# Kernel optimization log

Hardware: AMD Instinct MI355X
Metric: run time of the kernel (lower is better)

Reference implementation:

```python
import math
import jax, jax.numpy as jnp
import numpy as np

N = 8192
IN_DIM = 256
OUT_DIM = 128


def setup_inputs() -> dict:
    key = jax.random.key(0)
    k_feat, k_c, k_q, k_k, k_v = jax.random.split(key, 5)
    feat = jax.random.normal(k_feat, (N, IN_DIM), dtype=jnp.float32)
    counting_attn = jax.random.uniform(k_c, (N, N), dtype=jnp.float32)
    # Linear weights stored as [in_dim, out_dim] (x @ W == nn.Linear with W.T)
    Wq = jax.random.normal(k_q, (IN_DIM, OUT_DIM), dtype=jnp.float32) / math.sqrt(IN_DIM)
    Wk = jax.random.normal(k_k, (IN_DIM, OUT_DIM), dtype=jnp.float32) / math.sqrt(IN_DIM)
    Wv = jax.random.normal(k_v, (IN_DIM, OUT_DIM), dtype=jnp.float32) / math.sqrt(IN_DIM)
    return {"feat": feat, "bg": 0, "counting_attn": counting_attn,
            "Wq": Wq, "Wk": Wk, "Wv": Wv}


def reference(feat, bg, counting_attn, Wq, Wk, Wv):
    # bg (graph handle) is unused in the original forward; dropout prob = 0.
    Q = feat @ Wq                      # [N, D]
    K = feat @ Wk                      # [N, D]
    V = feat @ Wv                      # [N, D]
    scale = 1.0 / math.sqrt(Q.shape[1])
    logits = (Q @ K.T) * scale         # [N, N]
    logits = logits - jnp.max(logits, axis=1, keepdims=True)
    a_nomi = jnp.exp(logits) @ counting_attn          # [N, N]
    a_deno = jnp.sum(a_nomi, axis=1, keepdims=True)
    a_nor = a_nomi / (a_deno + 1e-9)
    ret = a_nor @ V                    # [N, D]
    return jax.nn.elu(ret)
```

## Files before the change

kernel.cpp:

```cpp
#include <hip/hip_runtime.h>


typedef __attribute__((ext_vector_type(8))) short bf16x8;
typedef __attribute__((ext_vector_type(4))) short bf16x4;
typedef __attribute__((ext_vector_type(4))) float f32x4;

#define SC2 (0.088388347648318447f * 1.4426950408889634f)

static __device__ __forceinline__ unsigned short f2bf(float f) {
    unsigned u = __float_as_uint(f);
    u = (u + 0x7fffu + ((u >> 16) & 1u)) >> 16;
    return (unsigned short)u;
}
static __device__ __forceinline__ float bf2f(unsigned short b) {
    return __uint_as_float(((unsigned)b) << 16);
}
static __device__ __forceinline__ unsigned pkbf(float lo, float hi) {
    unsigned r;
    asm("v_cvt_pk_bf16_f32 %0, %1, %2" : "=v"(r) : "v"(lo), "v"(hi));
    return r;
}
static __device__ __forceinline__ float fexp2(float x) {
    float r;
    asm("v_exp_f32 %0, %1" : "=v"(r) : "v"(x));
    return r;
}
static __device__ __forceinline__ bf16x8 pack8(const float4& a, const float4& b) {
    union { unsigned u[4]; bf16x8 v; } o;
    o.u[0] = pkbf(a.x, a.y); o.u[1] = pkbf(a.z, a.w);
    o.u[2] = pkbf(b.x, b.y); o.u[3] = pkbf(b.z, b.w);
    return o.v;
}
static __device__ __forceinline__ void gl_lds16(const unsigned short* g, unsigned short* l) {
    __builtin_amdgcn_global_load_lds(
        (const __attribute__((address_space(1))) unsigned int*)g,
        (__attribute__((address_space(3))) unsigned int*)l, 16, 0, 0);
}

__global__ __launch_bounds__(512) void qkv_mfma(
    const float* __restrict__ feat, const float* __restrict__ Wq,
    const float* __restrict__ Wk, const float* __restrict__ Wv,
    unsigned short* __restrict__ Qb, unsigned short* __restrict__ Kb,
    unsigned short* __restrict__ VbT, float* __restrict__ qn2,
    unsigned* __restrict__ knmax) {
    __shared__ unsigned short As[64][264];
    __shared__ unsigned short Bs[128][264];
    __shared__ float sn[2][64];
    const int tid = threadIdx.x;
    const int m0 = blockIdx.x * 64;
    const int mat = blockIdx.y;
    const float* W = (mat == 0) ? Wq : (mat == 1) ? Wk : Wv;
    const int lane = tid & 63, wv = tid >> 6;
    const int wm = wv & 3, wn = wv >> 2;
    const int ln15 = lane & 15, quad = lane >> 4;

    #pragma unroll
    for (int i = 0; i < 4; i++) {
        int s = tid + i * 512;
        int r = s >> 5, c8 = s & 31;
        const float* p = feat + (size_t)(m0 + r) * 256 + c8 * 8;
        const float4 f0 = *(const float4*)p;
        const float4 f1 = *(const float4*)(p + 4);
        *(bf16x8*)&As[r][c8 * 8] = pack8(f0, f1);
    }
    #pragma unroll
    for (int i = 0; i < 16; i++) {
        int s = tid + i * 512;
        int k = s >> 5, n4 = (s & 31) * 4;
        const float4 f = *(const float4*)(W + (size_t)k * 128 + n4);
        Bs[n4 + 0][k] = f2bf(f.x); Bs[n4 + 1][k] = f2bf(f.y);
        Bs[n4 + 2][k] = f2bf(f.z); Bs[n4 + 3][k] = f2bf(f.w);
    }
    __syncthreads();

    f32x4 acc[4];
    #pragma unroll
    for (int t = 0; t < 4; t++) acc[t] = f32x4{0.f, 0.f, 0.f, 0.f};
    #pragma unroll
    for (int ks = 0; ks < 8; ks++) {
        bf16x8 af = *(const bf16x8*)&As[wm * 16 + ln15][ks * 32 + quad * 8];
        #pragma unroll
        for (int t = 0; t < 4; t++) {
            bf16x8 bf = *(const bf16x8*)&Bs[wn * 64 + t * 16 + ln15][ks * 32 + quad * 8];
            acc[t] = __builtin_amdgcn_mfma_f32_16x16x32_bf16(af, bf, acc[t], 0, 0, 0);
        }
    }
    #pragma unroll
    for (int t = 0; t < 4; t++) {
        int n = wn * 64 + t * 16 + ln15;
        int mb = m0 + wm * 16 + quad * 4;
        if (mat == 2) {
            uint2 w;
            w.x = pkbf(acc[t][0], acc[t][1]);
            w.y = pkbf(acc[t][2], acc[t][3]);
            *(uint2*)(VbT + (size_t)n * 8192 + mb) = w;
        } else {
            unsigned short* dst = (mat == 0) ? Qb : Kb;
            #pragma unroll
            for (int reg = 0; reg < 4; reg++)
                dst[(size_t)(mb + reg) * 128 + n] = f2bf(acc[t][reg]);
        }
    }
    if (mat == 2) {
        #pragma unroll
        for (int i = 0; i < 8; i++) {
            int idx = tid + i * 512;
            int rr = idx >> 6, c = idx & 63;
            VbT[(size_t)(128 + rr) * 8192 + m0 + c] =
                (rr == 0) ? (unsigned short)0x3F80 : (unsigned short)0;
        }
    } else {
        float s[4];
        #pragma unroll
        for (int reg = 0; reg < 4; reg++) {
            float x = acc[0][reg] * acc[0][reg] + acc[1][reg] * acc[1][reg]
                    + acc[2][reg] * acc[2][reg] + acc[3][reg] * acc[3][reg];
            #pragma unroll
            for (int m = 1; m < 16; m <<= 1) x += __shfl_xor(x, m, 64);
            s[reg] = x;
        }
        if (ln15 == 0) {
            #pragma unroll
            for (int reg = 0; reg < 4; reg++)
                sn[wn][wm * 16 + quad * 4 + reg] = s[reg];
        }
        __syncthreads();
        if (tid < 64) {
            float tot = sn[0][tid] + sn[1][tid];
            if (mat == 0) {
                qn2[m0 + tid] = tot;
            } else {
                #pragma unroll
                for (int m = 1; m < 64; m <<= 1)
                    tot = fmaxf(tot, __shfl_xor(tot, m, 64));
                if (tid == 0) atomicMax(knmax, __float_as_uint(tot));
            }
        }
    }
}

__global__ __launch_bounds__(256, 4) void cv_kernel(
    const float* __restrict__ C, const unsigned short* __restrict__ VbT,
    float* __restrict__ CVpart) {
    __shared__ unsigned short As[64 * 64];
    __shared__ unsigned short Bs[192 * 64];
    const int tid = threadIdx.x;
    const int rg = blockIdx.x >> 3, sp = blockIdx.x & 7;
    const int m0 = rg * 64;
    const int k0 = sp * 1024;
    const int lane = tid & 63, wv = tid >> 6;
    const int mh = wv & 1, h2 = wv >> 1;
    const int ln15 = lane & 15, quad = lane >> 4;

    const int r0 = tid >> 3, gc = tid & 7;
    const int gsw = gc ^ (r0 & 7);
    const float* A0 = C + (size_t)(m0 + r0) * 8192 + k0 + gc * 8;
    const float* A1 = A0 + (size_t)32 * 8192;

    float4 pa[4];
    pa[0] = *(const float4*)A0; pa[1] = *(const float4*)(A0 + 4);
    pa[2] = *(const float4*)A1; pa[3] = *(const float4*)(A1 + 4);

    f32x4 acc[2][5];
    #pragma unroll
    for (int mt = 0; mt < 2; mt++)
        #pragma unroll
        for (int t = 0; t < 5; t++) acc[mt][t] = f32x4{0.f, 0.f, 0.f, 0.f};

    const int ra0 = mh * 32 + ln15;
    const int ra1 = mh * 32 + 16 + ln15;

    for (int c = 0; c < 16; c++) {
        __syncthreads();
        *(bf16x8*)&As[r0 * 64 + gsw * 8]        = pack8(pa[0], pa[1]);
        *(bf16x8*)&As[(r0 + 32) * 64 + gsw * 8] = pack8(pa[2], pa[3]);
        #pragma unroll
        for (int i = 0; i < 6; i++) {
            int s = (i * 4 + wv) * 64 + lane;
            int r = s >> 3, g = (s & 7) ^ (r & 7);
            gl_lds16(VbT + (size_t)r * 8192 + k0 + c * 64 + g * 8,
                     &Bs[(i * 4 + wv) * 512]);
        }
        asm volatile("" ::: "memory");
        if (c + 1 < 16) {
            const float* p0 = A0 + (c + 1) * 64;
            const float* p1 = A1 + (c + 1) * 64;
            pa[0] = *(const float4*)p0; pa[1] = *(const float4*)(p0 + 4);
            pa[2] = *(const float4*)p1; pa[3] = *(const float4*)(p1 + 4);
            asm volatile("s_waitcnt vmcnt(4) lgkmcnt(0)" ::: "memory");
        } else {
            asm volatile("s_waitcnt vmcnt(0) lgkmcnt(0)" ::: "memory");
        }
        __builtin_amdgcn_s_barrier();
        __builtin_amdgcn_sched_barrier(0);
        #pragma unroll
        for (int k2 = 0; k2 < 2; k2++) {
            const int lg = k2 * 4 + quad;
            bf16x8 a0 = *(const bf16x8*)&As[ra0 * 64 + ((lg ^ (ra0 & 7)) * 8)];
            bf16x8 a1 = *(const bf16x8*)&As[ra1 * 64 + ((lg ^ (ra1 & 7)) * 8)];
            #pragma unroll
            for (int t = 0; t < 5; t++) {
                int n = h2 * 80 + t * 16 + ln15;
                bf16x8 bf = *(const bf16x8*)&Bs[n * 64 + ((lg ^ (n & 7)) * 8)];
                acc[0][t] = __builtin_amdgcn_mfma_f32_16x16x32_bf16(a0, bf, acc[0][t], 0, 0, 0);
                acc[1][t] = __builtin_amdgcn_mfma_f32_16x16x32_bf16(a1, bf, acc[1][t], 0, 0, 0);
            }
        }
    }
    float* dst = CVpart + (size_t)sp * 160 * 8192;
    #pragma unroll
    for (int mt = 0; mt < 2; mt++)
        #pragma unroll
        for (int t = 0; t < 5; t++) {
            int n = h2 * 80 + t * 16 + ln15;
            int m = m0 + mh * 32 + mt * 16 + quad * 4;
            float4 w;
            w.x = acc[mt][t][0]; w.y = acc[mt][t][1];
            w.z = acc[mt][t][2]; w.w = acc[mt][t][3];
            *(float4*)(dst + (size_t)n * 8192 + m) = w;
        }
}

__global__ __launch_bounds__(256) void cvreduce_kernel(
    const float* __restrict__ CVpart, unsigned short* __restrict__ CVbT) {
    const size_t STR = (size_t)160 * 8192;
    int idx = blockIdx.x * 256 + threadIdx.x;
    const float* p = CVpart + (size_t)idx * 4;
    float4 s = *(const float4*)p;
    #pragma unroll
    for (int j = 1; j < 8; j++) {
        const float4 q = *(const float4*)(p + j * STR);
        s.x += q.x; s.y += q.y; s.z += q.z; s.w += q.w;
    }
    uint2 w;
    w.x = pkbf(s.x, s.y); w.y = pkbf(s.z, s.w);
    *(uint2*)(CVbT + (size_t)idx * 4) = w;
}

__global__ __launch_bounds__(256, 2) void flash_kernel(
    const unsigned short* __restrict__ Qb, const unsigned short* __restrict__ Kb,
    const unsigned short* __restrict__ CVbT, const float* __restrict__ qn2,
    const unsigned* __restrict__ knmax, float* __restrict__ Opart) {
    __shared__ unsigned short Ks[64 * 128];
    __shared__ unsigned short Cs[160 * 64];
    __shared__ unsigned short Ps[64][68];
    const int tid = threadIdx.x;
    const int rg = blockIdx.x >> 2, sp = blockIdx.x & 3;
    const int i0 = rg * 64;
    const int k0 = sp * 2048;
    const int lane = tid & 63, wv = tid >> 6;
    const int ln15 = lane & 15, quad = lane >> 4;
    const int p2 = wv & 1;
    const int h2 = wv >> 1;

    bf16x8 qf[2][4];
    #pragma unroll
    for (int mt = 0; mt < 2; mt++)
        #pragma unroll
        for (int kk = 0; kk < 4; kk++) {
            int row = i0 + p2 * 32 + mt * 16 + ln15;
            qf[mt][kk] = *(const bf16x8*)(Qb + (size_t)row * 128 + kk * 32 + quad * 8);
        }
    const float kn2 = __uint_as_float(*knmax);
    float Msr[2][4];
    #pragma unroll
    for (int mt = 0; mt < 2; mt++)
        #pragma unroll
        for (int reg = 0; reg < 4; reg++) {
            int row = p2 * 32 + mt * 16 + quad * 4 + reg;
            Msr[mt][reg] = sqrtf(qn2[i0 + row] * kn2) * SC2;
        }

    f32x4 acc[2][5];
    #pragma unroll
    for (int mt = 0; mt < 2; mt++)
        #pragma unroll
        for (int t = 0; t < 5; t++) acc[mt][t] = f32x4{0.f, 0.f, 0.f, 0.f};

    #pragma unroll
    for (int i = 0; i < 4; i++) {
        int s = (i * 4 + wv) * 64 + lane;
        int r = s >> 4, g = (s & 15) ^ (r & 15);
        gl_lds16(Kb + (size_t)(k0 + r) * 128 + g * 8, &Ks[(i * 4 + wv) * 512]);
    }

    for (int c = 0; c < 32; c++) {
        const int kb = k0 + c * 64;
        asm volatile("s_waitcnt vmcnt(0) lgkmcnt(0)" ::: "memory");
        __builtin_amdgcn_s_barrier();
        __builtin_amdgcn_sched_barrier(0);

        #pragma unroll
        for (int i = 0; i < 5; i++) {
            int s = (i * 4 + wv) * 64 + lane;
            int r = s >> 3, g = (s & 7) ^ (r & 7);
            gl_lds16(CVbT + (size_t)r * 8192 + kb + g * 8, &Cs[(i * 4 + wv) * 512]);
        }
        __builtin_amdgcn_sched_barrier(0);

        f32x4 pacc[2][2];
        #pragma unroll
        for (int mt = 0; mt < 2; mt++)
            #pragma unroll
            for (int kt = 0; kt < 2; kt++) pacc[mt][kt] = f32x4{0.f, 0.f, 0.f, 0.f};
        #pragma unroll
        for (int kk = 0; kk < 4; kk++) {
            #pragma unroll
            for (int kt = 0; kt < 2; kt++) {
                int r = h2 * 32 + kt * 16 + ln15;
                int lg = kk * 4 + quad;
                bf16x8 bk = *(const bf16x8*)&Ks[r * 128 + ((lg ^ (r & 15)) * 8)];
                pacc[0][kt] = __builtin_amdgcn_mfma_f32_16x16x32_bf16(qf[0][kk], bk, pacc[0][kt], 0, 0, 0);
                pacc[1][kt] = __builtin_amdgcn_mfma_f32_16x16x32_bf16(qf[1][kk], bk, pacc[1][kt], 0, 0, 0);
            }
        }
        #pragma unroll
        for (int mt = 0; mt < 2; mt++)
            #pragma unroll
            for (int kt = 0; kt < 2; kt++) {
                int key = h2 * 32 + kt * 16 + ln15;
                int row0 = p2 * 32 + mt * 16 + quad * 4;
                float e0 = fexp2(pacc[mt][kt][0] * SC2 - Msr[mt][0]);
                float e1 = fexp2(pacc[mt][kt][1] * SC2 - Msr[mt][1]);
                float e2 = fexp2(pacc[mt][kt][2] * SC2 - Msr[mt][2]);
                float e3 = fexp2(pacc[mt][kt][3] * SC2 - Msr[mt][3]);
                unsigned p01 = pkbf(e0, e1), p23 = pkbf(e2, e3);
                Ps[row0 + 0][key] = (unsigned short)(p01 & 0xffffu);
                Ps[row0 + 1][key] = (unsigned short)(p01 >> 16);
                Ps[row0 + 2][key] = (unsigned short)(p23 & 0xffffu);
                Ps[row0 + 3][key] = (unsigned short)(p23 >> 16);
            }

        asm volatile("s_waitcnt vmcnt(0) lgkmcnt(0)" ::: "memory");
        __builtin_amdgcn_s_barrier();
        __builtin_amdgcn_sched_barrier(0);

        if (c + 1 < 32) {
            const int kb2 = k0 + (c + 1) * 64;
            #pragma unroll
            for (int i = 0; i < 4; i++) {
                int s = (i * 4 + wv) * 64 + lane;
                int r = s >> 4, g = (s & 15) ^ (r & 15);
                gl_lds16(Kb + (size_t)(kb2 + r) * 128 + g * 8, &Ks[(i * 4 + wv) * 512]);
            }
        }
        __builtin_amdgcn_sched_barrier(0);

        #pragma unroll
        for (int ks = 0; ks < 2; ks++) {
            bf16x4 lo0 = *(const bf16x4*)&Ps[p2 * 32 + ln15][ks * 32 + quad * 8];
            bf16x4 hi0 = *(const bf16x4*)&Ps[p2 * 32 + ln15][ks * 32 + quad * 8 + 4];
            bf16x4 lo1 = *(const bf16x4*)&Ps[p2 * 32 + 16 + ln15][ks * 32 + quad * 8];
            bf16x4 hi1 = *(const bf16x4*)&Ps[p2 * 32 + 16 + ln15][ks * 32 + quad * 8 + 4];
            bf16x8 ap0, ap1;
            #pragma unroll
            for (int j = 0; j < 4; j++) {
                ap0[j] = lo0[j]; ap0[j + 4] = hi0[j];
                ap1[j] = lo1[j]; ap1[j + 4] = hi1[j];
            }
            #pragma unroll
            for (int t = 0; t < 5; t++) {
                int n = h2 * 80 + t * 16 + ln15;
                int lg = ks * 4 + quad;
                bf16x8 bc = *(const bf16x8*)&Cs[n * 64 + ((lg ^ (n & 7)) * 8)];
                acc[0][t] = __builtin_amdgcn_mfma_f32_16x16x32_bf16(ap0, bc, acc[0][t], 0, 0, 0);
                acc[1][t] = __builtin_amdgcn_mfma_f32_16x16x32_bf16(ap1, bc, acc[1][t], 0, 0, 0);
            }
        }
    }
    float* dst = Opart + (size_t)sp * 8192 * 160;
    #pragma unroll
    for (int mt = 0; mt < 2; mt++)
        #pragma unroll
        for (int t = 0; t < 5; t++)
            #pragma unroll
            for (int reg = 0; reg < 4; reg++) {
                int row = i0 + p2 * 32 + mt * 16 + quad * 4 + reg;
                int n = h2 * 80 + t * 16 + ln15;
                dst[(size_t)row * 160 + n] = acc[mt][t][reg];
            }
}

__global__ __launch_bounds__(256) void finalize_kernel(
    const float* __restrict__ Opart, float* __restrict__ out) {
    const size_t STR = (size_t)8192 * 160;
    int idx = blockIdx.x * 256 + threadIdx.x;
    int i = idx >> 7, n = idx & 127;
    const float* p = Opart + (size_t)i * 160;
    float val = 0.f, deno = 0.f;
    #pragma unroll
    for (int sp = 0; sp < 4; sp++) {
        val  += p[sp * STR + n];
        deno += p[sp * STR + 128];
    }
    float v = val / (deno + 1e-9f);
    out[idx] = (v > 0.f) ? v : expm1f(v);
}

extern "C" void kernel_launch(void* const* d_in, const int* in_sizes, int n_in,
                              void* d_out, int out_size, void* d_ws, size_t ws_size,
                              hipStream_t stream) {
    const float* feat = (const float*)d_in[0];
    const float* C    = (const float*)d_in[2];
    const float* Wq   = (const float*)d_in[3];
    const float* Wk   = (const float*)d_in[4];
    const float* Wv   = (const float*)d_in[5];
    float* out = (float*)d_out;

    char* ws = (char*)d_ws;
    unsigned short* Qb    = (unsigned short*)(ws + 0);
    unsigned short* Kb    = (unsigned short*)(ws + 2097152);
    unsigned short* VbT   = (unsigned short*)(ws + 4194304);
    float*          CVpart= (float*)(ws + 7340032);
    unsigned short* CVbT  = (unsigned short*)(ws + 49283072);
    float*          Opart = (float*)(ws + 51904512);
    float*          qn2   = (float*)(ws + 93847552);
    unsigned*       knmax = (unsigned*)(ws + 93880320);

    hipMemsetAsync(knmax, 0, 4, stream);
    qkv_mfma<<<dim3(128, 3), 512, 0, stream>>>(feat, Wq, Wk, Wv, Qb, Kb, VbT, qn2, knmax);
    cv_kernel<<<1024, 256, 0, stream>>>(C, VbT, CVpart);
    cvreduce_kernel<<<1280, 256, 0, stream>>>(CVpart, CVbT);
    flash_kernel<<<512, 256, 0, stream>>>(Qb, Kb, CVbT, qn2, knmax, Opart);
    finalize_kernel<<<4096, 256, 0, stream>>>(Opart, out);
}
```

Baseline: 486.8 us.

## Retile CV GEMM to 32-row blocks with 2-way split-K; transpose P tile in flash

The C·V kernel now uses 32-row tiles with a 2-way K split instead of 64 rows with an 8-way split. This shrinks the partial buffer and the reduction to two reads per element, but each block now reloads the V^T tile for fewer rows, and there are fewer blocks and less MFMA work per LDS load. Separately, the flash kernel swaps the MFMA operands so each lane holds one query row's scores. P can then be written with packed 64-bit swizzled LDS stores and read back as two 64-bit loads, instead of scattered 16-bit stores and element shuffles.

```diff
diff --git a/kernel.cpp b/kernel.cpp
--- a/kernel.cpp
+++ b/kernel.cpp
@@ -2,7 +2,6 @@
 
 
 typedef __attribute__((ext_vector_type(8))) short bf16x8;
-typedef __attribute__((ext_vector_type(4))) short bf16x4;
 typedef __attribute__((ext_vector_type(4))) float f32x4;
 
 #define SC2 (0.088388347648318447f * 1.4426950408889634f)
@@ -11,9 +10,6 @@
     unsigned u = __float_as_uint(f);
     u = (u + 0x7fffu + ((u >> 16) & 1u)) >> 16;
     return (unsigned short)u;
-}
-static __device__ __forceinline__ float bf2f(unsigned short b) {
-    return __uint_as_float(((unsigned)b) << 16);
 }
 static __device__ __forceinline__ unsigned pkbf(float lo, float hi) {
     unsigned r;
@@ -139,15 +135,15 @@
     }
 }
 
-__global__ __launch_bounds__(256, 4) void cv_kernel(
+__global__ __launch_bounds__(256, 2) void cv_kernel(
     const float* __restrict__ C, const unsigned short* __restrict__ VbT,
     float* __restrict__ CVpart) {
-    __shared__ unsigned short As[64 * 64];
+    __shared__ unsigned short As[32 * 64];
     __shared__ unsigned short Bs[192 * 64];
     const int tid = threadIdx.x;
-    const int rg = blockIdx.x >> 3, sp = blockIdx.x & 7;
-    const int m0 = rg * 64;
-    const int k0 = sp * 1024;
+    const int rg = blockIdx.x >> 1, sp = blockIdx.x & 1;
+    const int m0 = rg * 32;
+    const int k0 = sp * 4096;
     const int lane = tid & 63, wv = tid >> 6;
     const int mh = wv & 1, h2 = wv >> 1;
     const int ln15 = lane & 15, quad = lane >> 4;
@@ -155,25 +151,19 @@
     const int r0 = tid >> 3, gc = tid & 7;
     const int gsw = gc ^ (r0 & 7);
     const float* A0 = C + (size_t)(m0 + r0) * 8192 + k0 + gc * 8;
-    const float* A1 = A0 + (size_t)32 * 8192;
-
-    float4 pa[4];
+
+    float4 pa[2];
     pa[0] = *(const float4*)A0; pa[1] = *(const float4*)(A0 + 4);
-    pa[2] = *(const float4*)A1; pa[3] = *(const float4*)(A1 + 4);
-
-    f32x4 acc[2][5];
-    #pragma unroll
-    for (int mt = 0; mt < 2; mt++)
-        #pragma unroll
-        for (int t = 0; t < 5; t++) acc[mt][t] = f32x4{0.f, 0.f, 0.f, 0.f};
-
-    const int ra0 = mh * 32 + ln15;
-    const int ra1 = mh * 32 + 16 + ln15;
-
-    for (int c = 0; c < 16; c++) {
+
+    f32x4 acc[5];
+    #pragma unroll
+    for (int t = 0; t < 5; t++) acc[t] = f32x4{0.f, 0.f, 0.f, 0.f};
+
+    const int ra = mh * 16 + ln15;
+
+    for (int c = 0; c < 64; c++) {
         __syncthreads();
-        *(bf16x8*)&As[r0 * 64 + gsw * 8]        = pack8(pa[0], pa[1]);
-        *(bf16x8*)&As[(r0 + 32) * 64 + gsw * 8] = pack8(pa[2], pa[3]);
+        *(bf16x8*)&As[r0 * 64 + gsw * 8] = pack8(pa[0], pa[1]);
         #pragma unroll
         for (int i = 0; i < 6; i++) {
             int s = (i * 4 + wv) * 64 + lane;
@@ -182,12 +172,10 @@
                      &Bs[(i * 4 + wv) * 512]);
         }
         asm volatile("" ::: "memory");
-        if (c + 1 < 16) {
+        if (c + 1 < 64) {
             const float* p0 = A0 + (c + 1) * 64;
-            const float* p1 = A1 + (c + 1) * 64;
             pa[0] = *(const float4*)p0; pa[1] = *(const float4*)(p0 + 4);
-            pa[2] = *(const float4*)p1; pa[3] = *(const float4*)(p1 + 4);
-            asm volatile("s_waitcnt vmcnt(4) lgkmcnt(0)" ::: "memory");
+            asm volatile("s_waitcnt vmcnt(2) lgkmcnt(0)" ::: "memory");
         } else {
             asm volatile("s_waitcnt vmcnt(0) lgkmcnt(0)" ::: "memory");
         }
@@ -196,29 +184,25 @@
         #pragma unroll
         for (int k2 = 0; k2 < 2; k2++) {
             const int lg = k2 * 4 + quad;
-            bf16x8 a0 = *(const bf16x8*)&As[ra0 * 64 + ((lg ^ (ra0 & 7)) * 8)];
-            bf16x8 a1 = *(const bf16x8*)&As[ra1 * 64 + ((lg ^ (ra1 & 7)) * 8)];
+            bf16x8 a = *(const bf16x8*)&As[ra * 64 + ((lg ^ (ra & 7)) * 8)];
             #pragma unroll
             for (int t = 0; t < 5; t++) {
                 int n = h2 * 80 + t * 16 + ln15;
                 bf16x8 bf = *(const bf16x8*)&Bs[n * 64 + ((lg ^ (n & 7)) * 8)];
-                acc[0][t] = __builtin_amdgcn_mfma_f32_16x16x32_bf16(a0, bf, acc[0][t], 0, 0, 0);
-                acc[1][t] = __builtin_amdgcn_mfma_f32_16x16x32_bf16(a1, bf, acc[1][t], 0, 0, 0);
+                acc[t] = __builtin_amdgcn_mfma_f32_16x16x32_bf16(a, bf, acc[t], 0, 0, 0);
             }
         }
     }
     float* dst = CVpart + (size_t)sp * 160 * 8192;
     #pragma unroll
-    for (int mt = 0; mt < 2; mt++)
-        #pragma unroll
-        for (int t = 0; t < 5; t++) {
-            int n = h2 * 80 + t * 16 + ln15;
-            int m = m0 + mh * 32 + mt * 16 + quad * 4;
-            float4 w;
-            w.x = acc[mt][t][0]; w.y = acc[mt][t][1];
-            w.z = acc[mt][t][2]; w.w = acc[mt][t][3];
-            *(float4*)(dst + (size_t)n * 8192 + m) = w;
-        }
+    for (int t = 0; t < 5; t++) {
+        int n = h2 * 80 + t * 16 + ln15;
+        int m = m0 + mh * 16 + quad * 4;
+        float4 w;
+        w.x = acc[t][0]; w.y = acc[t][1];
+        w.z = acc[t][2]; w.w = acc[t][3];
+        *(float4*)(dst + (size_t)n * 8192 + m) = w;
+    }
 }
 
 __global__ __launch_bounds__(256) void cvreduce_kernel(
@@ -227,11 +211,8 @@
     int idx = blockIdx.x * 256 + threadIdx.x;
     const float* p = CVpart + (size_t)idx * 4;
     float4 s = *(const float4*)p;
-    #pragma unroll
-    for (int j = 1; j < 8; j++) {
-        const float4 q = *(const float4*)(p + j * STR);
-        s.x += q.x; s.y += q.y; s.z += q.z; s.w += q.w;
-    }
+    const float4 q = *(const float4*)(p + STR);
+    s.x += q.x; s.y += q.y; s.z += q.z; s.w += q.w;
     uint2 w;
     w.x = pkbf(s.x, s.y); w.y = pkbf(s.z, s.w);
     *(uint2*)(CVbT + (size_t)idx * 4) = w;
@@ -243,7 +224,7 @@
     const unsigned* __restrict__ knmax, float* __restrict__ Opart) {
     __shared__ unsigned short Ks[64 * 128];
     __shared__ unsigned short Cs[160 * 64];
-    __shared__ unsigned short Ps[64][68];
+    __shared__ unsigned Ps2[64 * 32];
     const int tid = threadIdx.x;
     const int rg = blockIdx.x >> 2, sp = blockIdx.x & 3;
     const int i0 = rg * 64;
@@ -252,6 +233,7 @@
     const int ln15 = lane & 15, quad = lane >> 4;
     const int p2 = wv & 1;
     const int h2 = wv >> 1;
+    const int xr = ln15 << 1;
 
     bf16x8 qf[2][4];
     #pragma unroll
@@ -262,14 +244,10 @@
             qf[mt][kk] = *(const bf16x8*)(Qb + (size_t)row * 128 + kk * 32 + quad * 8);
         }
     const float kn2 = __uint_as_float(*knmax);
-    float Msr[2][4];
+    float Msr2[2];
     #pragma unroll
     for (int mt = 0; mt < 2; mt++)
-        #pragma unroll
-        for (int reg = 0; reg < 4; reg++) {
-            int row = p2 * 32 + mt * 16 + quad * 4 + reg;
-            Msr[mt][reg] = sqrtf(qn2[i0 + row] * kn2) * SC2;
-        }
+        Msr2[mt] = sqrtf(qn2[i0 + p2 * 32 + mt * 16 + ln15] * kn2) * SC2;
 
     f32x4 acc[2][5];
     #pragma unroll
@@ -310,26 +288,24 @@
                 int r = h2 * 32 + kt * 16 + ln15;
                 int lg = kk * 4 + quad;
                 bf16x8 bk = *(const bf16x8*)&Ks[r * 128 + ((lg ^ (r & 15)) * 8)];
-                pacc[0][kt] = __builtin_amdgcn_mfma_f32_16x16x32_bf16(qf[0][kk], bk, pacc[0][kt], 0, 0, 0);
-                pacc[1][kt] = __builtin_amdgcn_mfma_f32_16x16x32_bf16(qf[1][kk], bk, pacc[1][kt], 0, 0, 0);
-            }
-        }
-        #pragma unroll
-        for (int mt = 0; mt < 2; mt++)
+                pacc[0][kt] = __builtin_amdgcn_mfma_f32_16x16x32_bf16(bk, qf[0][kk], pacc[0][kt], 0, 0, 0);
+                pacc[1][kt] = __builtin_amdgcn_mfma_f32_16x16x32_bf16(bk, qf[1][kk], pacc[1][kt], 0, 0, 0);
+            }
+        }
+        #pragma unroll
+        for (int mt = 0; mt < 2; mt++) {
+            const int row = p2 * 32 + mt * 16 + ln15;
             #pragma unroll
             for (int kt = 0; kt < 2; kt++) {
-                int key = h2 * 32 + kt * 16 + ln15;
-                int row0 = p2 * 32 + mt * 16 + quad * 4;
-                float e0 = fexp2(pacc[mt][kt][0] * SC2 - Msr[mt][0]);
-                float e1 = fexp2(pacc[mt][kt][1] * SC2 - Msr[mt][1]);
-                float e2 = fexp2(pacc[mt][kt][2] * SC2 - Msr[mt][2]);
-                float e3 = fexp2(pacc[mt][kt][3] * SC2 - Msr[mt][3]);
-                unsigned p01 = pkbf(e0, e1), p23 = pkbf(e2, e3);
-                Ps[row0 + 0][key] = (unsigned short)(p01 & 0xffffu);
-                Ps[row0 + 1][key] = (unsigned short)(p01 >> 16);
-                Ps[row0 + 2][key] = (unsigned short)(p23 & 0xffffu);
-                Ps[row0 + 3][key] = (unsigned short)(p23 >> 16);
-            }
+                float e0 = fexp2(pacc[mt][kt][0] * SC2 - Msr2[mt]);
+                float e1 = fexp2(pacc[mt][kt][1] * SC2 - Msr2[mt]);
+                float e2 = fexp2(pacc[mt][kt][2] * SC2 - Msr2[mt]);
+                float e3 = fexp2(pacc[mt][kt][3] * SC2 - Msr2[mt]);
+                uint2 u; u.x = pkbf(e0, e1); u.y = pkbf(e2, e3);
+                int p0 = h2 * 16 + kt * 8 + quad * 2;
+                *(uint2*)&Ps2[row * 32 + (p0 ^ xr)] = u;
+            }
+        }
 
         asm volatile("s_waitcnt vmcnt(0) lgkmcnt(0)" ::: "memory");
         __builtin_amdgcn_s_barrier();
@@ -348,23 +324,21 @@
 
         #pragma unroll
         for (int ks = 0; ks < 2; ks++) {
-            bf16x4 lo0 = *(const bf16x4*)&Ps[p2 * 32 + ln15][ks * 32 + quad * 8];
-            bf16x4 hi0 = *(const bf16x4*)&Ps[p2 * 32 + ln15][ks * 32 + quad * 8 + 4];
-            bf16x4 lo1 = *(const bf16x4*)&Ps[p2 * 32 + 16 + ln15][ks * 32 + quad * 8];
-            bf16x4 hi1 = *(const bf16x4*)&Ps[p2 * 32 + 16 + ln15][ks * 32 + quad * 8 + 4];
-            bf16x8 ap0, ap1;
-            #pragma unroll
-            for (int j = 0; j < 4; j++) {
-                ap0[j] = lo0[j]; ap0[j + 4] = hi0[j];
-                ap1[j] = lo1[j]; ap1[j + 4] = hi1[j];
-            }
+            const int ba = ks * 16 + quad * 4;
+            const int rowa = (p2 * 32 + ln15) * 32;
+            const int rowb = rowa + 16 * 32;
+            union { uint2 d[2]; bf16x8 v; } A0, A1;
+            A0.d[0] = *(const uint2*)&Ps2[rowa + ((ba    ) ^ xr)];
+            A0.d[1] = *(const uint2*)&Ps2[rowa + ((ba + 2) ^ xr)];
+            A1.d[0] = *(const uint2*)&Ps2[rowb + ((ba    ) ^ xr)];
+            A1.d[1] = *(const uint2*)&Ps2[rowb + ((ba + 2) ^ xr)];
             #pragma unroll
             for (int t = 0; t < 5; t++) {
                 int n = h2 * 80 + t * 16 + ln15;
                 int lg = ks * 4 + quad;
                 bf16x8 bc = *(const bf16x8*)&Cs[n * 64 + ((lg ^ (n & 7)) * 8)];
-                acc[0][t] = __builtin_amdgcn_mfma_f32_16x16x32_bf16(ap0, bc, acc[0][t], 0, 0, 0);
-                acc[1][t] = __builtin_amdgcn_mfma_f32_16x16x32_bf16(ap1, bc, acc[1][t], 0, 0, 0);
+                acc[0][t] = __builtin_amdgcn_mfma_f32_16x16x32_bf16(A0.v, bc, acc[0][t], 0, 0, 0);
+                acc[1][t] = __builtin_amdgcn_mfma_f32_16x16x32_bf16(A1.v, bc, acc[1][t], 0, 0, 0);
             }
         }
     }
@@ -419,7 +393,7 @@
 
     hipMemsetAsync(knmax, 0, 4, stream);
     qkv_mfma<<<dim3(128, 3), 512, 0, stream>>>(feat, Wq, Wk, Wv, Qb, Kb, VbT, qn2, knmax);
-    cv_kernel<<<1024, 256, 0, stream>>>(C, VbT, CVpart);
+    cv_kernel<<<512, 256, 0, stream>>>(C, VbT, CVpart);
     cvreduce_kernel<<<1280, 256, 0, stream>>>(CVpart, CVbT);
     flash_kernel<<<512, 256, 0, stream>>>(Qb, Kb, CVbT, qn2, knmax, Opart);
     finalize_kernel<<<4096, 256, 0, stream>>>(Opart, out);
```

Result: no change. 493.7 us (+1.4%).
